# Kernel tuning notes

Measured on AMD Instinct MI355X. Metric: run time of the kernel, lower is better.

The kernel has to match this reference:

```python
import jax, jax.numpy as jnp
from jax import lax
import numpy as np

V, D, H, K = 50000, 300, 256, 37  # vocab, emb dim, lstm hidden, num_tags
B, T = 64, 256


def setup_inputs() -> dict:
    key = jax.random.key(0)
    ks = jax.random.split(key, 24)
    lengths = jax.random.randint(ks[0], (B,), T // 2, T + 1)
    valid = jnp.arange(T)[None, :] < lengths[:, None]
    text = jnp.where(valid, jax.random.randint(ks[1], (B, T), 1, V), 0)
    sbj = jax.random.randint(ks[2], (B, T), 0, K)

    def p(k, shape, s=0.05):
        return jax.random.normal(k, shape, jnp.float32) * s

    return {
        "text": text, "sbj": sbj,
        "emb": p(ks[3], (V, D), 0.1),
        # layer 0 (input D=300), forward + backward directions, torch gate order i,f,g,o
        "Wih0f": p(ks[4], (4 * H, D)), "Whh0f": p(ks[5], (4 * H, H)), "b0f": jnp.zeros((4 * H,), jnp.float32),
        "Wih0b": p(ks[6], (4 * H, D)), "Whh0b": p(ks[7], (4 * H, H)), "b0b": jnp.zeros((4 * H,), jnp.float32),
        # layer 1 (input 2H=512)
        "Wih1f": p(ks[8], (4 * H, 2 * H)), "Whh1f": p(ks[9], (4 * H, H)), "b1f": jnp.zeros((4 * H,), jnp.float32),
        "Wih1b": p(ks[10], (4 * H, 2 * H)), "Whh1b": p(ks[11], (4 * H, H)), "b1b": jnp.zeros((4 * H,), jnp.float32),
        "W_sbj": p(ks[12], (K, 2 * H)), "b_sbj": jnp.zeros((K,), jnp.float32),
        # CRF params (torchcrf init: uniform(-0.1, 0.1))
        "start_t": p(ks[13], (K,), 0.1), "end_t": p(ks[14], (K,), 0.1), "trans": p(ks[15], (K, K), 0.1),
    }


def _lstm(x, Wih, Whh, b, reverse):
    # x: [T, B, Din] time-major; returns hidden states [T, B, H]
    Bn, Hn = x.shape[1], Whh.shape[1]

    def step(carry, xt):
        h, c = carry
        z = xt @ Wih.T + h @ Whh.T + b
        i, f, g, o = jnp.split(z, 4, axis=-1)
        c = jax.nn.sigmoid(f) * c + jax.nn.sigmoid(i) * jnp.tanh(g)
        h = jax.nn.sigmoid(o) * jnp.tanh(c)
        return (h, c), h

    init = (jnp.zeros((Bn, Hn), x.dtype), jnp.zeros((Bn, Hn), x.dtype))
    return lax.scan(step, init, x, reverse=reverse)[1]


def reference(text, sbj, emb, Wih0f, Whh0f, b0f, Wih0b, Whh0b, b0b,
              Wih1f, Whh1f, b1f, Wih1b, Whh1b, b1b,
              W_sbj, b_sbj, start_t, end_t, trans):
    mask = (text != 0)                      # [B, T]
    x = jnp.transpose(emb[text], (1, 0, 2))  # [T, B, D]
    h0 = jnp.concatenate([_lstm(x, Wih0f, Whh0f, b0f, False),
                          _lstm(x, Wih0b, Whh0b, b0b, True)], axis=-1)   # [T, B, 2H]
    h1 = jnp.concatenate([_lstm(h0, Wih1f, Whh1f, b1f, False),
                          _lstm(h0, Wih1b, Whh1b, b1b, True)], axis=-1)  # [T, B, 2H]
    em = h1 @ W_sbj.T + b_sbj               # emissions [T, B, K]

    tags = sbj.T                            # [T, B]
    m = mask.T                              # [T, B]
    mf = m.astype(em.dtype)

    # --- numerator: score of the gold path ---
    em_sel = jnp.take_along_axis(em, tags[:, :, None], axis=2)[..., 0]  # [T, B]
    tr_sel = trans[tags[:-1], tags[1:]]                                  # [T-1, B]
    seq_ends = m.sum(0) - 1
    last_tags = tags[seq_ends, jnp.arange(tags.shape[1])]
    num = (start_t[tags[0]] + em_sel[0]
           + jnp.sum((em_sel[1:] + tr_sel) * mf[1:], axis=0)
           + end_t[last_tags])              # [B]

    # --- log partition: forward algorithm (logsumexp DP over K tags) ---
    def step(score, inp):
        em_t, m_t = inp
        nxt = jax.scipy.special.logsumexp(
            score[:, :, None] + trans[None, :, :] + em_t[:, None, :], axis=1)
        return jnp.where(m_t[:, None], nxt, score), None

    score0 = start_t[None, :] + em[0]       # [B, K]
    score = lax.scan(step, score0, (em[1:], m[1:]))[0]
    logZ = jax.scipy.special.logsumexp(score + end_t[None, :], axis=-1)  # [B]

    llh = num - logZ
    return -(llh.sum() / mf.sum())          # -1 * token_mean log-likelihood
```

## Files before the change

### kernel.cpp

```cpp
#include <hip/hip_runtime.h>
#include <math.h>

#define TT 256
#define BB 64
#define DD 300
#define KP0 320
#define HH 256
#define KK 37
#define FH 1024
#define MTOT (TT*BB)

typedef __attribute__((ext_vector_type(8))) short short8;
typedef __attribute__((ext_vector_type(4))) float f32x4;

__device__ __forceinline__ float bf2f(unsigned short u) {
    union { float f; unsigned int i; } v; v.i = ((unsigned int)u) << 16; return v.f;
}
__device__ __forceinline__ unsigned short f2bf(float f) {
    union { float f; unsigned int i; } v; v.f = f;
    unsigned int i = v.i;
    unsigned int r = (i + 0x7FFFu + ((i >> 16) & 1u)) >> 16;
    return (unsigned short)r;
}
__device__ __forceinline__ float sigm(float x)   { return 1.0f / (1.0f + __expf(-x)); }
__device__ __forceinline__ float tanh_f(float x) { return 2.0f / (1.0f + __expf(-2.0f * x)) - 1.0f; }

__device__ __forceinline__ int sb0(int w) { return (w << 24) >> 24; }
__device__ __forceinline__ int sb1(int w) { return (w << 16) >> 24; }
__device__ __forceinline__ int sb2(int w) { return (w <<  8) >> 24; }
__device__ __forceinline__ int sb3(int w) { return  w        >> 24; }

#if defined(__has_builtin)
#if __has_builtin(__builtin_amdgcn_sdot4)
#define HAVE_SDOT4 1
#endif
#endif

__device__ __forceinline__ int dot4i8(int a, int b, int c) {
#ifdef HAVE_SDOT4
    return __builtin_amdgcn_sdot4(a, b, c, false);
#else
    return c + sb0(a) * sb0(b) + sb1(a) * sb1(b) + sb2(a) * sb2(b) + sb3(a) * sb3(b);
#endif
}

__device__ __forceinline__ void lstm_dot(int hw, int4 wv, int& a0, int& a1, int& a2, int& a3) {
    a0 = dot4i8(hw, wv.x, a0);
    a1 = dot4i8(hw, wv.y, a1);
    a2 = dot4i8(hw, wv.z, a2);
    a3 = dot4i8(hw, wv.w, a3);
}

__device__ __forceinline__ void barrier_lgkm() {
    asm volatile("s_waitcnt lgkmcnt(0)\n\ts_barrier" ::: "memory");
}

__device__ __forceinline__ int perm_col(int nn) { return ((nn & 255) << 2) | (nn >> 8); }

__global__ __launch_bounds__(64) void conv_scale(
    const float* __restrict__ w0f, const float* __restrict__ w0b,
    const float* __restrict__ w1f, const float* __restrict__ w1b,
    float* __restrict__ S)
{
    const int m = blockIdx.x >> 10;
    const int r = blockIdx.x & 1023;
    const float* W = m == 0 ? w0f : m == 1 ? w0b : m == 2 ? w1f : w1b;
    const int t = threadIdx.x;
    float mx = 0.f;
    for (int k = t; k < HH; k += 64) mx = fmaxf(mx, fabsf(W[r * HH + k]));
    #pragma unroll
    for (int s = 32; s > 0; s >>= 1) mx = fmaxf(mx, __shfl_down(mx, s, 64));
    if (t == 0) {
        const int g = r >> 8, u = r & 255;
        S[m * 1024 + u * 4 + g] = fmaxf(mx, 1e-20f) / 127.0f;
    }
}

__global__ __launch_bounds__(256) void conv_wq(
    const float* __restrict__ w0f, const float* __restrict__ w0b,
    const float* __restrict__ w1f, const float* __restrict__ w1b,
    const float* __restrict__ S, unsigned int* __restrict__ WQ)
{
    const int idx = blockIdx.x * 256 + threadIdx.x;
    const int m = idx >> 16;
    const int r = idx & 65535;
    const float* W = m == 0 ? w0f : m == 1 ? w0b : m == 2 ? w1f : w1b;
    const int g  = r & 3;
    const int u  = (r >> 2) & 255;
    const int j  = (r >> 10) & 15;
    const int kq = r >> 14;
    const int k0 = kq * 64 + j * 4;
    const float s = S[m * 1024 + u * 4 + g];
    const float4 wv = *(const float4*)(W + (g * HH + u) * HH + k0);
    int q0 = (int)rintf(wv.x / s), q1 = (int)rintf(wv.y / s);
    int q2 = (int)rintf(wv.z / s), q3 = (int)rintf(wv.w / s);
    q0 = max(-127, min(127, q0)); q1 = max(-127, min(127, q1));
    q2 = max(-127, min(127, q2)); q3 = max(-127, min(127, q3));
    WQ[idx] = (unsigned int)(q0 & 0xff) | ((unsigned int)(q1 & 0xff) << 8) |
              ((unsigned int)(q2 & 0xff) << 16) | ((unsigned int)(q3 & 0xff) << 24);
}

__global__ __launch_bounds__(256) void conv_wsbj_bf(
    const float* __restrict__ Wsbj, unsigned short* __restrict__ WB)
{
    const int idx = blockIdx.x * 256 + threadIdx.x;
    if (idx >= 64 * 512) return;
    const int r = idx >> 9, cidx = idx & 511;
    WB[idx] = (r < KK) ? f2bf(Wsbj[r * 512 + cidx]) : (unsigned short)0;
}

__global__ __launch_bounds__(320) void conv_gather(
    const int* __restrict__ text, const float* __restrict__ emb,
    unsigned short* __restrict__ Abf)
{
    const int r = blockIdx.x;
    const int k = threadIdx.x;
    const int t = r >> 6, b = r & 63;
    const int idx = text[b * TT + t];
    Abf[r * KP0 + k] = (k < DD) ? f2bf(emb[(size_t)idx * DD + k]) : (unsigned short)0;
}

__global__ __launch_bounds__(256) void conv_w4(
    const float* __restrict__ s0, const float* __restrict__ s1,
    const float* __restrict__ s2, const float* __restrict__ s3,
    unsigned short* __restrict__ d0, unsigned short* __restrict__ d1,
    unsigned short* __restrict__ d2, unsigned short* __restrict__ d3)
{
    const int z = blockIdx.y;
    const float* src = z == 0 ? s0 : z == 1 ? s1 : z == 2 ? s2 : s3;
    unsigned short* dst = z == 0 ? d0 : z == 1 ? d1 : z == 2 ? d2 : d3;
    const int kin   = z < 2 ? DD  : 512;
    const int kout  = z < 2 ? KP0 : 512;
    const int total = 1024 * kout;
    const int idx = blockIdx.x * 256 + threadIdx.x;
    if (idx >= total) return;
    const int rr = idx / kout, k = idx - rr * kout;
    dst[idx] = (k < kin) ? f2bf(src[rr * kin + k]) : (unsigned short)0;
}

__global__ __launch_bounds__(256) void gemm_mfma2(
    const unsigned short* __restrict__ A,
    const unsigned short* __restrict__ Wf,
    const unsigned short* __restrict__ Wb,
    const float* __restrict__ biasf,
    const float* __restrict__ biasb,
    unsigned short* __restrict__ outf,
    unsigned short* __restrict__ outb,
    int lda)
{
    const unsigned short* W = blockIdx.z ? Wb : Wf;
    const float* bias        = blockIdx.z ? biasb : biasf;
    unsigned short* out      = blockIdx.z ? outb : outf;

    const int bm = blockIdx.x * 128;
    const int bn = blockIdx.y * 128;
    const int tid = threadIdx.x;
    const int lane = tid & 63;
    const int wave = tid >> 6;
    const int wm = (wave & 1) * 64;
    const int wn = (wave >> 1) * 64;

    __shared__ __align__(16) unsigned short As[128 * 32];
    __shared__ __align__(16) unsigned short Bs[128 * 32];

    f32x4 acc[4][4] = {};

    const int srow = tid >> 2;
    const int sk = (tid & 3) * 8;

    const unsigned short* ga0 = A + (size_t)(bm + srow) * lda + sk;
    const unsigned short* ga1 = A + (size_t)(bm + srow + 64) * lda + sk;
    const unsigned short* gb0 = W + (size_t)(bn + srow) * lda + sk;
    const unsigned short* gb1 = W + (size_t)(bn + srow + 64) * lda + sk;

    unsigned short* lA0 = As + wave * 512;
    unsigned short* lA1 = As + 2048 + wave * 512;
    unsigned short* lB0 = Bs + wave * 512;
    unsigned short* lB1 = Bs + 2048 + wave * 512;

    const int kiters = lda >> 5;
    for (int kb = 0; kb < kiters; kb++) {
        const int k0 = kb * 32;
        __builtin_amdgcn_global_load_lds(
            (const __attribute__((address_space(1))) unsigned int*)(ga0 + k0),
            (__attribute__((address_space(3))) unsigned int*)lA0, 16, 0, 0);
        __builtin_amdgcn_global_load_lds(
            (const __attribute__((address_space(1))) unsigned int*)(ga1 + k0),
            (__attribute__((address_space(3))) unsigned int*)lA1, 16, 0, 0);
        __builtin_amdgcn_global_load_lds(
            (const __attribute__((address_space(1))) unsigned int*)(gb0 + k0),
            (__attribute__((address_space(3))) unsigned int*)lB0, 16, 0, 0);
        __builtin_amdgcn_global_load_lds(
            (const __attribute__((address_space(1))) unsigned int*)(gb1 + k0),
            (__attribute__((address_space(3))) unsigned int*)lB1, 16, 0, 0);
        __syncthreads();

        short8 af[4], bfr[4];
        #pragma unroll
        for (int i = 0; i < 4; i++) {
            af[i]  = *(const short8*)&As[(wm + i * 16 + (lane & 15)) * 32 + (lane >> 4) * 8];
            bfr[i] = *(const short8*)&Bs[(wn + i * 16 + (lane & 15)) * 32 + (lane >> 4) * 8];
        }
        #pragma unroll
        for (int i = 0; i < 4; i++)
            #pragma unroll
            for (int j = 0; j < 4; j++)
                acc[i][j] = __builtin_amdgcn_mfma_f32_16x16x32_bf16(af[i], bfr[j], acc[i][j], 0, 0, 0);
        __syncthreads();
    }

    const int cn = lane & 15;
    const int cr = (lane >> 4) * 4;
    #pragma unroll
    for (int j = 0; j < 4; j++) {
        const int n = bn + wn + j * 16 + cn;
        const float bv = bias[n];
        const int pc = perm_col(n);
        #pragma unroll
        for (int i = 0; i < 4; i++) {
            #pragma unroll
            for (int r = 0; r < 4; r++) {
                const int m = bm + wm + i * 16 + cr + r;
                out[(size_t)m * FH + pc] = f2bf(acc[i][j][r] + bv);
            }
        }
    }
}

__global__ __launch_bounds__(256) void gemm_em(
    const unsigned short* __restrict__ A,
    const unsigned short* __restrict__ W,
    const float* __restrict__ bias,
    float* __restrict__ em)
{
    const int bm = blockIdx.x * 128;
    const int tid = threadIdx.x;
    const int lane = tid & 63;
    const int wave = tid >> 6;
    const int wm = (wave & 1) * 64;
    const int wn = (wave >> 1) * 32;

    __shared__ __align__(16) unsigned short As[128 * 32];
    __shared__ __align__(16) unsigned short Bs[64 * 32];

    f32x4 acc[4][2] = {};

    const int srow = tid >> 2;
    const int sk = (tid & 3) * 8;

    const unsigned short* ga0 = A + (size_t)(bm + srow) * 512 + sk;
    const unsigned short* ga1 = A + (size_t)(bm + srow + 64) * 512 + sk;
    const unsigned short* gb  = W + (size_t)srow * 512 + sk;

    unsigned short* lA0 = As + wave * 512;
    unsigned short* lA1 = As + 2048 + wave * 512;
    unsigned short* lB  = Bs + wave * 512;

    for (int kb = 0; kb < 16; kb++) {
        const int k0 = kb * 32;
        __builtin_amdgcn_global_load_lds(
            (const __attribute__((address_space(1))) unsigned int*)(ga0 + k0),
            (__attribute__((address_space(3))) unsigned int*)lA0, 16, 0, 0);
        __builtin_amdgcn_global_load_lds(
            (const __attribute__((address_space(1))) unsigned int*)(ga1 + k0),
            (__attribute__((address_space(3))) unsigned int*)lA1, 16, 0, 0);
        __builtin_amdgcn_global_load_lds(
            (const __attribute__((address_space(1))) unsigned int*)(gb + k0),
            (__attribute__((address_space(3))) unsigned int*)lB, 16, 0, 0);
        __syncthreads();

        short8 af[4], bfr[2];
        #pragma unroll
        for (int i = 0; i < 4; i++)
            af[i]  = *(const short8*)&As[(wm + i * 16 + (lane & 15)) * 32 + (lane >> 4) * 8];
        #pragma unroll
        for (int j = 0; j < 2; j++)
            bfr[j] = *(const short8*)&Bs[(wn + j * 16 + (lane & 15)) * 32 + (lane >> 4) * 8];
        #pragma unroll
        for (int i = 0; i < 4; i++)
            #pragma unroll
            for (int j = 0; j < 2; j++)
                acc[i][j] = __builtin_amdgcn_mfma_f32_16x16x32_bf16(af[i], bfr[j], acc[i][j], 0, 0, 0);
        __syncthreads();
    }

    const int cn = lane & 15;
    const int cr = (lane >> 4) * 4;
    #pragma unroll
    for (int j = 0; j < 2; j++) {
        const int n = wn + j * 16 + cn;
        if (n < KK) {
            const float bv = bias[n];
            #pragma unroll
            for (int i = 0; i < 4; i++) {
                #pragma unroll
                for (int r = 0; r < 4; r++) {
                    const int m = bm + wm + i * 16 + cr + r;
                    em[(size_t)m * KK + n] = acc[i][j][r] + bv;
                }
            }
        }
    }
}

__global__ __launch_bounds__(1024, 4) void lstm_kernel(
    const unsigned short* __restrict__ zin_f, const unsigned short* __restrict__ zin_b,
    const int* __restrict__ WQf, const int* __restrict__ WQb,
    const float* __restrict__ Sf, const float* __restrict__ Sb,
    unsigned short* __restrict__ h_out)
{
    const int dir = blockIdx.y;
    const unsigned short* zin = dir ? zin_b : zin_f;
    const int*   WQ = dir ? WQb : WQf;
    const float* S  = dir ? Sb  : Sf;
    const int off = dir ? HH : 0;

    const int b = blockIdx.x;
    const int tid = threadIdx.x;
    const int u  = tid & 255;
    const int kq = tid >> 8;

    __shared__ __align__(16) unsigned char hq8[2][HH];
    __shared__ int4 red[3][HH];

    const int4* wp = (const int4*)WQ + kq * 16 * 256 + u;
    const int4 w0  = wp[ 0 * 256], w1  = wp[ 1 * 256], w2  = wp[ 2 * 256], w3  = wp[ 3 * 256];
    const int4 w4  = wp[ 4 * 256], w5  = wp[ 5 * 256], w6  = wp[ 6 * 256], w7  = wp[ 7 * 256];
    const int4 w8  = wp[ 8 * 256], w9  = wp[ 9 * 256], w10 = wp[10 * 256], w11 = wp[11 * 256];
    const int4 w12 = wp[12 * 256], w13 = wp[13 * 256], w14 = wp[14 * 256], w15 = wp[15 * 256];

    float4 sc = make_float4(0.f, 0.f, 0.f, 0.f);
    if (kq == 0) {
        sc = *(const float4*)(S + 4 * u);
        const float inv127 = 1.0f / 127.0f;
        sc.x *= inv127; sc.y *= inv127; sc.z *= inv127; sc.w *= inv127;
    }
    float c = 0.0f;
    int cur = 0;
    if (tid < 128) ((unsigned int*)hq8)[tid] = 0u;
    __syncthreads();

    ushort4 zv = make_ushort4(0, 0, 0, 0);
    if (kq == 0) {
        const int tt0 = dir ? (TT - 1) : 0;
        zv = *(const ushort4*)(zin + (tt0 * BB + b) * FH + 4 * u);
    }

    for (int ts = 0; ts < TT; ts++) {
        const int tt = dir ? (TT - 1 - ts) : ts;
        const int row = tt * BB + b;

        ushort4 zv_n = make_ushort4(0, 0, 0, 0);
        if (kq == 0) {
            const int ts_n = (ts + 1 < TT) ? (ts + 1) : ts;
            const int tt_n = dir ? (TT - 1 - ts_n) : ts_n;
            zv_n = *(const ushort4*)(zin + (tt_n * BB + b) * FH + 4 * u);
        }

        const int4* hv = (const int4*)&hq8[cur][kq * 64];
        const int4 hA = hv[0], hB = hv[1], hC = hv[2], hD = hv[3];

        int a0 = 0, a1 = 0, a2 = 0, a3 = 0;
        lstm_dot(hA.x, w0,  a0, a1, a2, a3);
        lstm_dot(hA.y, w1,  a0, a1, a2, a3);
        lstm_dot(hA.z, w2,  a0, a1, a2, a3);
        lstm_dot(hA.w, w3,  a0, a1, a2, a3);
        lstm_dot(hB.x, w4,  a0, a1, a2, a3);
        lstm_dot(hB.y, w5,  a0, a1, a2, a3);
        lstm_dot(hB.z, w6,  a0, a1, a2, a3);
        lstm_dot(hB.w, w7,  a0, a1, a2, a3);
        lstm_dot(hC.x, w8,  a0, a1, a2, a3);
        lstm_dot(hC.y, w9,  a0, a1, a2, a3);
        lstm_dot(hC.z, w10, a0, a1, a2, a3);
        lstm_dot(hC.w, w11, a0, a1, a2, a3);
        lstm_dot(hD.x, w12, a0, a1, a2, a3);
        lstm_dot(hD.y, w13, a0, a1, a2, a3);
        lstm_dot(hD.z, w14, a0, a1, a2, a3);
        lstm_dot(hD.w, w15, a0, a1, a2, a3);

        if (kq) red[kq - 1][u] = make_int4(a0, a1, a2, a3);
        barrier_lgkm();

        if (kq == 0) {
            const int4 r0 = red[0][u], r1 = red[1][u], r2 = red[2][u];
            const int A0 = a0 + r0.x + r1.x + r2.x;
            const int A1 = a1 + r0.y + r1.y + r2.y;
            const int A2 = a2 + r0.z + r1.z + r2.z;
            const int A3 = a3 + r0.w + r1.w + r2.w;
            const float zi  = (float)A0 * sc.x + bf2f(zv.x);
            const float zf_ = (float)A1 * sc.y + bf2f(zv.y);
            const float zg  = (float)A2 * sc.z + bf2f(zv.z);
            const float zo  = (float)A3 * sc.w + bf2f(zv.w);
            const float cc = sigm(zf_) * c + sigm(zi) * tanh_f(zg);
            c = cc;
            const float hh = sigm(zo) * tanh_f(cc);
            hq8[cur ^ 1][u] = (unsigned char)((int)rintf(hh * 127.0f));
            h_out[row * (2 * HH) + off + u] = f2bf(hh);
        }
        barrier_lgkm();
        cur ^= 1;
        zv = zv_n;
    }
}

__global__ __launch_bounds__(64) void crf_kernel(
    const int* __restrict__ text, const int* __restrict__ sbj,
    const float* __restrict__ em,
    const float* __restrict__ start_t, const float* __restrict__ end_t,
    const float* __restrict__ trans, float* __restrict__ accum)
{
    const int b = blockIdx.x;
    const int tid = threadIdx.x;
    __shared__ float tr[KK * KK];
    __shared__ float sc[2][KK];
    for (int x = tid; x < KK * KK; x += 64) tr[x] = trans[x];

    int cnt = 0;
    for (int t = tid; t < TT; t += 64) cnt += (text[b * TT + t] != 0) ? 1 : 0;
    #pragma unroll
    for (int s = 32; s > 0; s >>= 1) cnt += __shfl_down(cnt, s, 64);
    const int len = __shfl(cnt, 0, 64);

    __syncthreads();

    float part = 0.f;
    for (int t = tid; t < TT; t += 64) {
        if (t >= 1 && t < len) {
            const int tg = sbj[b * TT + t];
            const int tp = sbj[b * TT + t - 1];
            part += em[(t * BB + b) * KK + tg] + tr[tp * KK + tg];
        }
    }
    #pragma unroll
    for (int s = 32; s > 0; s >>= 1) part += __shfl_down(part, s, 64);

    float tc[KK];
    #pragma unroll
    for (int k1 = 0; k1 < KK; k1++) tc[k1] = (tid < KK) ? tr[k1 * KK + tid] : 0.f;

    if (tid < KK) sc[0][tid] = start_t[tid] + em[b * KK + tid];
    __syncthreads();
    int cur = 0;
    for (int t = 1; t < len; t++) {
        float nv = 0.f;
        if (tid < KK) {
            const float ev = em[(t * BB + b) * KK + tid];
            float v[KK];
            float mx = -1e30f;
            #pragma unroll
            for (int k1 = 0; k1 < KK; k1++) {
                v[k1] = sc[cur][k1] + tc[k1];
                mx = fmaxf(mx, v[k1]);
            }
            float s = 0.f;
            #pragma unroll
            for (int k1 = 0; k1 < KK; k1++)
                s += __expf(v[k1] - mx);
            nv = mx + __logf(s) + ev;
        }
        if (tid < KK) sc[cur ^ 1][tid] = nv;
        __syncthreads();
        cur ^= 1;
    }

    if (tid == 0) {
        const int tg0 = sbj[b * TT];
        const int tgl = sbj[b * TT + len - 1];
        const float num = start_t[tg0] + em[b * KK + tg0] + part + end_t[tgl];
        float mx = -1e30f;
        for (int k = 0; k < KK; k++) mx = fmaxf(mx, sc[cur][k] + end_t[k]);
        float s = 0.f;
        for (int k = 0; k < KK; k++) s += __expf(sc[cur][k] + end_t[k] - mx);
        const float logZ = mx + __logf(s);
        atomicAdd(&accum[0], num - logZ);
        atomicAdd(&accum[1], (float)len);
    }
}

__global__ void init_kernel(float* __restrict__ accum) {
    if (threadIdx.x < 2) accum[threadIdx.x] = 0.0f;
}
__global__ void final_kernel(const float* __restrict__ accum, float* __restrict__ out) {
    out[0] = -(accum[0] / accum[1]);
}

extern "C" void kernel_launch(void* const* d_in, const int* in_sizes, int n_in,
                              void* d_out, int out_size, void* d_ws, size_t ws_size,
                              hipStream_t stream)
{
    (void)in_sizes; (void)n_in; (void)out_size; (void)ws_size;
    const int*   text  = (const int*)d_in[0];
    const int*   sbj   = (const int*)d_in[1];
    const float* emb   = (const float*)d_in[2];
    const float* Wih0f = (const float*)d_in[3];
    const float* Whh0f = (const float*)d_in[4];
    const float* b0f   = (const float*)d_in[5];
    const float* Wih0b = (const float*)d_in[6];
    const float* Whh0b = (const float*)d_in[7];
    const float* b0b   = (const float*)d_in[8];
    const float* Wih1f = (const float*)d_in[9];
    const float* Whh1f = (const float*)d_in[10];
    const float* b1f   = (const float*)d_in[11];
    const float* Wih1b = (const float*)d_in[12];
    const float* Whh1b = (const float*)d_in[13];
    const float* b1b   = (const float*)d_in[14];
    const float* Wsbj  = (const float*)d_in[15];
    const float* bsbj  = (const float*)d_in[16];
    const float* start_t = (const float*)d_in[17];
    const float* end_t   = (const float*)d_in[18];
    const float* trans   = (const float*)d_in[19];

    char* ws = (char*)d_ws;
    unsigned short* zf   = (unsigned short*)(ws + 0);
    unsigned short* zb   = (unsigned short*)(ws + 33554432);
    unsigned short* h0   = (unsigned short*)(ws + 67108864);
    unsigned short* h1   = (unsigned short*)(ws + 83886080);
    unsigned short* Wb0f = (unsigned short*)(ws + 67108864);
    unsigned short* Wb0b = (unsigned short*)(ws + 67764224);
    unsigned short* Abf  = (unsigned short*)(ws + 83886080);
    unsigned short* Wb1f = (unsigned short*)(ws + 94371840);
    unsigned short* Wb1b = (unsigned short*)(ws + 95420416);
    unsigned int*   WQ   = (unsigned int*)(ws + 100663296);
    float*          Sq   = (float*)(ws + 101711872);
    unsigned short* WsbjB = (unsigned short*)(ws + 102760448);
    float*          acc  = (float*)(ws + 102836224);
    float*           em  = (float*)(ws + 0);
    float* out = (float*)d_out;

    const int* WQ0f = (const int*)(WQ + 0 * 65536);
    const int* WQ0b = (const int*)(WQ + 1 * 65536);
    const int* WQ1f = (const int*)(WQ + 2 * 65536);
    const int* WQ1b = (const int*)(WQ + 3 * 65536);
    const float* S0f = Sq + 0 * 1024;
    const float* S0b = Sq + 1 * 1024;
    const float* S1f = Sq + 2 * 1024;
    const float* S1b = Sq + 3 * 1024;

    init_kernel<<<1, 64, 0, stream>>>(acc);
    conv_scale<<<dim3(4096), 64, 0, stream>>>(Whh0f, Whh0b, Whh1f, Whh1b, Sq);
    conv_wq<<<dim3(1024), 256, 0, stream>>>(Whh0f, Whh0b, Whh1f, Whh1b, Sq, WQ);
    conv_wsbj_bf<<<dim3(128), 256, 0, stream>>>(Wsbj, WsbjB);
    conv_gather<<<dim3(MTOT), 320, 0, stream>>>(text, emb, Abf);
    conv_w4<<<dim3(2048, 4), 256, 0, stream>>>(Wih0f, Wih0b, Wih1f, Wih1b,
                                               Wb0f, Wb0b, Wb1f, Wb1b);

    gemm_mfma2<<<dim3(128, 8, 2), 256, 0, stream>>>(Abf, Wb0f, Wb0b, b0f, b0b, zf, zb, KP0);
    lstm_kernel<<<dim3(BB, 2), 1024, 0, stream>>>(zf, zb, WQ0f, WQ0b, S0f, S0b, h0);
    gemm_mfma2<<<dim3(128, 8, 2), 256, 0, stream>>>(h0, Wb1f, Wb1b, b1f, b1b, zf, zb, 512);
    lstm_kernel<<<dim3(BB, 2), 1024, 0, stream>>>(zf, zb, WQ1f, WQ1b, S1f, S1b, h1);

    gemm_em<<<dim3(128), 256, 0, stream>>>(h1, WsbjB, bsbj, em);
    crf_kernel<<<BB, 64, 0, stream>>>(text, sbj, em, start_t, end_t, trans, acc);
    final_kernel<<<1, 1, 0, stream>>>(acc, out);
}
```

Measured before the change: 968.9 us.

## Halve LSTM block size with wider per-thread K split, fuse weight quantization kernels

The LSTM recurrence kernel now runs 512 threads per block instead of 1024. Each thread holds 32 int4 weight registers covering half of the hidden dimension, so the cross-thread reduction goes from three partial sums to one. The two Whh quantization kernels are merged into a single kernel that computes the row scale and packs int8 weights in one pass. The CRF kernel prefetches the next emission value and uses a lighter barrier. The LSTM change trades more register pressure and longer serial dot chains per step for less shared-memory reduction and barrier cost.

```diff
diff --git a/kernel.cpp b/kernel.cpp
--- a/kernel.cpp
+++ b/kernel.cpp
@@ -57,47 +57,30 @@
 
 __device__ __forceinline__ int perm_col(int nn) { return ((nn & 255) << 2) | (nn >> 8); }
 
-__global__ __launch_bounds__(64) void conv_scale(
+__global__ __launch_bounds__(64) void conv_quant(
     const float* __restrict__ w0f, const float* __restrict__ w0b,
     const float* __restrict__ w1f, const float* __restrict__ w1b,
-    float* __restrict__ S)
+    float* __restrict__ S, unsigned int* __restrict__ WQ)
 {
     const int m = blockIdx.x >> 10;
     const int r = blockIdx.x & 1023;
     const float* W = m == 0 ? w0f : m == 1 ? w0b : m == 2 ? w1f : w1b;
     const int t = threadIdx.x;
-    float mx = 0.f;
-    for (int k = t; k < HH; k += 64) mx = fmaxf(mx, fabsf(W[r * HH + k]));
+    const float4 wv = *(const float4*)(W + r * HH + t * 4);
+    float mx = fmaxf(fmaxf(fabsf(wv.x), fabsf(wv.y)), fmaxf(fabsf(wv.z), fabsf(wv.w)));
     #pragma unroll
     for (int s = 32; s > 0; s >>= 1) mx = fmaxf(mx, __shfl_down(mx, s, 64));
-    if (t == 0) {
-        const int g = r >> 8, u = r & 255;
-        S[m * 1024 + u * 4 + g] = fmaxf(mx, 1e-20f) / 127.0f;
-    }
-}
-
-__global__ __launch_bounds__(256) void conv_wq(
-    const float* __restrict__ w0f, const float* __restrict__ w0b,
-    const float* __restrict__ w1f, const float* __restrict__ w1b,
-    const float* __restrict__ S, unsigned int* __restrict__ WQ)
-{
-    const int idx = blockIdx.x * 256 + threadIdx.x;
-    const int m = idx >> 16;
-    const int r = idx & 65535;
-    const float* W = m == 0 ? w0f : m == 1 ? w0b : m == 2 ? w1f : w1b;
-    const int g  = r & 3;
-    const int u  = (r >> 2) & 255;
-    const int j  = (r >> 10) & 15;
-    const int kq = r >> 14;
-    const int k0 = kq * 64 + j * 4;
-    const float s = S[m * 1024 + u * 4 + g];
-    const float4 wv = *(const float4*)(W + (g * HH + u) * HH + k0);
+    const float mxall = __shfl(mx, 0, 64);
+    const float s = fmaxf(mxall, 1e-20f) / 127.0f;
+    const int g = r >> 8, u = r & 255;
+    if (t == 0) S[m * 1024 + u * 4 + g] = s;
     int q0 = (int)rintf(wv.x / s), q1 = (int)rintf(wv.y / s);
     int q2 = (int)rintf(wv.z / s), q3 = (int)rintf(wv.w / s);
     q0 = max(-127, min(127, q0)); q1 = max(-127, min(127, q1));
     q2 = max(-127, min(127, q2)); q3 = max(-127, min(127, q3));
-    WQ[idx] = (unsigned int)(q0 & 0xff) | ((unsigned int)(q1 & 0xff) << 8) |
-              ((unsigned int)(q2 & 0xff) << 16) | ((unsigned int)(q3 & 0xff) << 24);
+    WQ[m * 65536 + (t * 256 + u) * 4 + g] =
+        (unsigned int)(q0 & 0xff) | ((unsigned int)(q1 & 0xff) << 8) |
+        ((unsigned int)(q2 & 0xff) << 16) | ((unsigned int)(q3 & 0xff) << 24);
 }
 
 __global__ __launch_bounds__(256) void conv_wsbj_bf(
@@ -303,7 +286,7 @@
     }
 }
 
-__global__ __launch_bounds__(1024, 4) void lstm_kernel(
+__global__ __launch_bounds__(512, 2) void lstm_kernel(
     const unsigned short* __restrict__ zin_f, const unsigned short* __restrict__ zin_b,
     const int* __restrict__ WQf, const int* __restrict__ WQb,
     const float* __restrict__ Sf, const float* __restrict__ Sb,
@@ -318,19 +301,18 @@
     const int b = blockIdx.x;
     const int tid = threadIdx.x;
     const int u  = tid & 255;
-    const int kq = tid >> 8;
+    const int kh = tid >> 8;
 
     __shared__ __align__(16) unsigned char hq8[2][HH];
-    __shared__ int4 red[3][HH];
-
-    const int4* wp = (const int4*)WQ + kq * 16 * 256 + u;
-    const int4 w0  = wp[ 0 * 256], w1  = wp[ 1 * 256], w2  = wp[ 2 * 256], w3  = wp[ 3 * 256];
-    const int4 w4  = wp[ 4 * 256], w5  = wp[ 5 * 256], w6  = wp[ 6 * 256], w7  = wp[ 7 * 256];
-    const int4 w8  = wp[ 8 * 256], w9  = wp[ 9 * 256], w10 = wp[10 * 256], w11 = wp[11 * 256];
-    const int4 w12 = wp[12 * 256], w13 = wp[13 * 256], w14 = wp[14 * 256], w15 = wp[15 * 256];
+    __shared__ int4 red[HH];
+
+    const int4* wp = (const int4*)WQ + kh * 32 * 256 + u;
+    int4 w[32];
+    #pragma unroll
+    for (int j = 0; j < 32; j++) w[j] = wp[j * 256];
 
     float4 sc = make_float4(0.f, 0.f, 0.f, 0.f);
-    if (kq == 0) {
+    if (kh == 0) {
         sc = *(const float4*)(S + 4 * u);
         const float inv127 = 1.0f / 127.0f;
         sc.x *= inv127; sc.y *= inv127; sc.z *= inv127; sc.w *= inv127;
@@ -341,7 +323,7 @@
     __syncthreads();
 
     ushort4 zv = make_ushort4(0, 0, 0, 0);
-    if (kq == 0) {
+    if (kh == 0) {
         const int tt0 = dir ? (TT - 1) : 0;
         zv = *(const ushort4*)(zin + (tt0 * BB + b) * FH + 4 * u);
     }
@@ -351,42 +333,32 @@
         const int row = tt * BB + b;
 
         ushort4 zv_n = make_ushort4(0, 0, 0, 0);
-        if (kq == 0) {
+        if (kh == 0) {
             const int ts_n = (ts + 1 < TT) ? (ts + 1) : ts;
             const int tt_n = dir ? (TT - 1 - ts_n) : ts_n;
             zv_n = *(const ushort4*)(zin + (tt_n * BB + b) * FH + 4 * u);
         }
 
-        const int4* hv = (const int4*)&hq8[cur][kq * 64];
-        const int4 hA = hv[0], hB = hv[1], hC = hv[2], hD = hv[3];
-
+        const int4* hv = (const int4*)&hq8[cur][kh * 128];
         int a0 = 0, a1 = 0, a2 = 0, a3 = 0;
-        lstm_dot(hA.x, w0,  a0, a1, a2, a3);
-        lstm_dot(hA.y, w1,  a0, a1, a2, a3);
-        lstm_dot(hA.z, w2,  a0, a1, a2, a3);
-        lstm_dot(hA.w, w3,  a0, a1, a2, a3);
-        lstm_dot(hB.x, w4,  a0, a1, a2, a3);
-        lstm_dot(hB.y, w5,  a0, a1, a2, a3);
-        lstm_dot(hB.z, w6,  a0, a1, a2, a3);
-        lstm_dot(hB.w, w7,  a0, a1, a2, a3);
-        lstm_dot(hC.x, w8,  a0, a1, a2, a3);
-        lstm_dot(hC.y, w9,  a0, a1, a2, a3);
-        lstm_dot(hC.z, w10, a0, a1, a2, a3);
-        lstm_dot(hC.w, w11, a0, a1, a2, a3);
-        lstm_dot(hD.x, w12, a0, a1, a2, a3);
-        lstm_dot(hD.y, w13, a0, a1, a2, a3);
-        lstm_dot(hD.z, w14, a0, a1, a2, a3);
-        lstm_dot(hD.w, w15, a0, a1, a2, a3);
-
-        if (kq) red[kq - 1][u] = make_int4(a0, a1, a2, a3);
+        #pragma unroll
+        for (int jq = 0; jq < 8; jq++) {
+            const int4 hw = hv[jq];
+            lstm_dot(hw.x, w[4 * jq + 0], a0, a1, a2, a3);
+            lstm_dot(hw.y, w[4 * jq + 1], a0, a1, a2, a3);
+            lstm_dot(hw.z, w[4 * jq + 2], a0, a1, a2, a3);
+            lstm_dot(hw.w, w[4 * jq + 3], a0, a1, a2, a3);
+        }
+
+        if (kh) red[u] = make_int4(a0, a1, a2, a3);
         barrier_lgkm();
 
-        if (kq == 0) {
-            const int4 r0 = red[0][u], r1 = red[1][u], r2 = red[2][u];
-            const int A0 = a0 + r0.x + r1.x + r2.x;
-            const int A1 = a1 + r0.y + r1.y + r2.y;
-            const int A2 = a2 + r0.z + r1.z + r2.z;
-            const int A3 = a3 + r0.w + r1.w + r2.w;
+        if (kh == 0) {
+            const int4 r0 = red[u];
+            const int A0 = a0 + r0.x;
+            const int A1 = a1 + r0.y;
+            const int A2 = a2 + r0.z;
+            const int A3 = a3 + r0.w;
             const float zi  = (float)A0 * sc.x + bf2f(zv.x);
             const float zf_ = (float)A1 * sc.y + bf2f(zv.y);
             const float zg  = (float)A2 * sc.z + bf2f(zv.z);
@@ -441,10 +413,11 @@
     if (tid < KK) sc[0][tid] = start_t[tid] + em[b * KK + tid];
     __syncthreads();
     int cur = 0;
+    float ev = (tid < KK && len > 1) ? em[(BB + b) * KK + tid] : 0.f;
     for (int t = 1; t < len; t++) {
+        const float ev_n = (tid < KK && t + 1 < len) ? em[((t + 1) * BB + b) * KK + tid] : 0.f;
         float nv = 0.f;
         if (tid < KK) {
-            const float ev = em[(t * BB + b) * KK + tid];
             float v[KK];
             float mx = -1e30f;
             #pragma unroll
@@ -459,8 +432,9 @@
             nv = mx + __logf(s) + ev;
         }
         if (tid < KK) sc[cur ^ 1][tid] = nv;
-        __syncthreads();
+        barrier_lgkm();
         cur ^= 1;
+        ev = ev_n;
     }
 
     if (tid == 0) {
@@ -537,17 +511,16 @@
     const float* S1b = Sq + 3 * 1024;
 
     init_kernel<<<1, 64, 0, stream>>>(acc);
-    conv_scale<<<dim3(4096), 64, 0, stream>>>(Whh0f, Whh0b, Whh1f, Whh1b, Sq);
-    conv_wq<<<dim3(1024), 256, 0, stream>>>(Whh0f, Whh0b, Whh1f, Whh1b, Sq, WQ);
+    conv_quant<<<dim3(4096), 64, 0, stream>>>(Whh0f, Whh0b, Whh1f, Whh1b, Sq, WQ);
     conv_wsbj_bf<<<dim3(128), 256, 0, stream>>>(Wsbj, WsbjB);
     conv_gather<<<dim3(MTOT), 320, 0, stream>>>(text, emb, Abf);
     conv_w4<<<dim3(2048, 4), 256, 0, stream>>>(Wih0f, Wih0b, Wih1f, Wih1b,
                                                Wb0f, Wb0b, Wb1f, Wb1b);
 
     gemm_mfma2<<<dim3(128, 8, 2), 256, 0, stream>>>(Abf, Wb0f, Wb0b, b0f, b0b, zf, zb, KP0);
-    lstm_kernel<<<dim3(BB, 2), 1024, 0, stream>>>(zf, zb, WQ0f, WQ0b, S0f, S0b, h0);
+    lstm_kernel<<<dim3(BB, 2), 512, 0, stream>>>(zf, zb, WQ0f, WQ0b, S0f, S0b, h0);
     gemm_mfma2<<<dim3(128, 8, 2), 256, 0, stream>>>(h0, Wb1f, Wb1b, b1f, b1b, zf, zb, 512);
-    lstm_kernel<<<dim3(BB, 2), 1024, 0, stream>>>(zf, zb, WQ1f, WQ1b, S1f, S1b, h1);
+    lstm_kernel<<<dim3(BB, 2), 512, 0, stream>>>(zf, zb, WQ1f, WQ1b, S1f, S1b, h1);
 
     gemm_em<<<dim3(128), 256, 0, stream>>>(h1, WsbjB, bsbj, em);
     crf_kernel<<<BB, 64, 0, stream>>>(text, sbj, em, start_t, end_t, trans, acc);
```

New measurement: 972.1 us. About the same (+0.3%).
